# Performance work log

Hardware: AMD Instinct MI355X
Metric: run time of the kernel (lower is better)

The kernel has to match this reference:

```python
import jax, jax.numpy as jnp
import numpy as np

N_ITEMS = 100000
EMBED_DIM = 128
N_SESSIONS = 16384
TOTAL_ITEMS = 819200


def setup_inputs() -> dict:
    key = jax.random.key(0)
    k1, k2, k3 = jax.random.split(key, 3)
    embeddings = jax.random.normal(k1, (N_ITEMS, EMBED_DIM), dtype=jnp.float32)
    item_ids = jax.random.randint(k2, (TOTAL_ITEMS,), 0, N_ITEMS, dtype=jnp.int64)
    segment_ids = jnp.sort(jax.random.randint(k3, (TOTAL_ITEMS,), 0, N_SESSIONS, dtype=jnp.int64))
    return {"embeddings": embeddings, "item_ids": item_ids,
            "segment_ids": segment_ids, "num_sessions": N_SESSIONS}


def reference(embeddings, item_ids, segment_ids, num_sessions):
    # Ragged per-session mean of gathered item embeddings
    gathered = embeddings[item_ids]                      # [total_items, d]
    sums = jax.ops.segment_sum(gathered, segment_ids, num_segments=num_sessions)
    counts = jax.ops.segment_sum(jnp.ones((item_ids.shape[0],), dtype=embeddings.dtype),
                                 segment_ids, num_segments=num_sessions)
    counts = jnp.maximum(counts, 1.0)                    # guard empty sessions
    return sums / counts[:, None]                        # [num_sessions, d]
```

## Files before the change

kernel.cpp:

```cpp
#include <hip/hip_runtime.h>
#include <hip/hip_fp16.h>


constexpr int D = 128;
constexpr int IDS_CAP = 4096;

typedef float f32x2 __attribute__((ext_vector_type(2)));

__global__ void find_starts_diff(const int* __restrict__ seg, int total,
                                 int nsess, int* __restrict__ starts) {
    int j = blockIdx.x * blockDim.x + threadIdx.x;
    if (j >= total) return;
    const int cur  = seg[j];
    const int prev = (j == 0) ? -1 : seg[j - 1];
    for (int s = prev + 1; s <= cur; ++s) starts[s] = j;
    if (j == total - 1) {
        for (int s = cur + 1; s <= nsess; ++s) starts[s] = total;
    }
}

__global__ __launch_bounds__(256)
void repack_kernel(const float* __restrict__ emb, __half* __restrict__ emb2,
                   int nitems) {
    const int item = blockIdx.x * 4 + (threadIdx.x >> 6);
    if (item >= nitems) return;
    const int lane = threadIdx.x & 63;
    const f32x2 v = __builtin_nontemporal_load(
        reinterpret_cast<const f32x2*>(emb + (size_t)item * D) + lane);
    const __half2 h = __floats2half2_rn(v.x, v.y);
    const int g = lane >> 3;
    const int o = lane & 7;
    __half2* dst = reinterpret_cast<__half2*>(
        emb2 + (size_t)g * nitems * 16 + (size_t)item * 16);
    dst[o] = h;
}

__global__ __launch_bounds__(256)
void gather_mean_octet(const __half* __restrict__ emb2,
                       const int* __restrict__ ids,
                       const int* __restrict__ starts,
                       float* __restrict__ out,
                       int nitems, int nsess) {
    __shared__ int lds_ids[IDS_CAP];

    const int g    = blockIdx.x & 7;
    const int s0   = (blockIdx.x >> 3) * 32;
    const int sidx = s0 + (threadIdx.x >> 3);
    const int dl   = threadIdx.x & 7;

    const int sEnd  = (s0 + 32 < nsess) ? s0 + 32 : nsess;
    const int base0 = starts[s0];
    const int range = starts[sEnd] - base0;
    const bool use_lds = (range <= IDS_CAP);

    if (use_lds) {
        for (int t = threadIdx.x; t < range; t += 256)
            lds_ids[t] = ids[base0 + t];
    }
    __syncthreads();

    if (sidx >= nsess) return;

    const int beg = starts[sidx];
    const int len = starts[sidx + 1] - beg;

    const __half* p = emb2 + (size_t)g * nitems * 16 + dl * 2;

    float ax = 0.f, ay = 0.f;

    if (use_lds) {
        const int* idp = lds_ids + (beg - base0);
        int j = 0;
        for (; j + 8 <= len; j += 8) {
            int id[8];
            #pragma unroll
            for (int k = 0; k < 8; ++k) id[k] = idp[j + k];
            float2 f[8];
            #pragma unroll
            for (int k = 0; k < 8; ++k)
                f[k] = __half22float2(
                    *reinterpret_cast<const __half2*>(p + (size_t)id[k] * 16));
            #pragma unroll
            for (int k = 0; k < 8; ++k) { ax += f[k].x; ay += f[k].y; }
        }
        for (; j < len; ++j) {
            const float2 f = __half22float2(
                *reinterpret_cast<const __half2*>(p + (size_t)idp[j] * 16));
            ax += f.x; ay += f.y;
        }
    } else {
        const int* idp = ids + beg;
        int j = 0;
        for (; j + 4 <= len; j += 4) {
            const int i0 = idp[j + 0];
            const int i1 = idp[j + 1];
            const int i2 = idp[j + 2];
            const int i3 = idp[j + 3];
            const float2 f0 = __half22float2(*reinterpret_cast<const __half2*>(p + (size_t)i0 * 16));
            const float2 f1 = __half22float2(*reinterpret_cast<const __half2*>(p + (size_t)i1 * 16));
            const float2 f2 = __half22float2(*reinterpret_cast<const __half2*>(p + (size_t)i2 * 16));
            const float2 f3 = __half22float2(*reinterpret_cast<const __half2*>(p + (size_t)i3 * 16));
            ax += f0.x + f1.x + f2.x + f3.x;
            ay += f0.y + f1.y + f2.y + f3.y;
        }
        for (; j < len; ++j) {
            const float2 f = __half22float2(
                *reinterpret_cast<const __half2*>(p + (size_t)idp[j] * 16));
            ax += f.x; ay += f.y;
        }
    }

    const float inv = (len > 0) ? 1.0f / (float)len : 0.0f;
    f32x2 o = {ax * inv, ay * inv};
    *reinterpret_cast<f32x2*>(out + (size_t)sidx * D + g * 16 + dl * 2) = o;
}

__global__ __launch_bounds__(256)
void seg_mean_kernel(const float* __restrict__ emb,
                     const int* __restrict__ ids,
                     const int* __restrict__ starts,
                     float* __restrict__ out, int nsess) {
    const int tid  = threadIdx.x;
    const int s    = blockIdx.x * 4 + (tid >> 6);
    if (s >= nsess) return;
    const int lane = tid & 63;
    const int gq   = lane >> 5;
    const int l32  = lane & 31;

    const int beg = starts[s];
    const int end = starts[s + 1];

    float4 acc = make_float4(0.f, 0.f, 0.f, 0.f);
    for (int j = beg + gq; j < end; j += 2) {
        const int id = ids[j];
        const float4 v = reinterpret_cast<const float4*>(emb + (size_t)id * D)[l32];
        acc.x += v.x; acc.y += v.y; acc.z += v.z; acc.w += v.w;
    }
    acc.x += __shfl_down(acc.x, 32);
    acc.y += __shfl_down(acc.y, 32);
    acc.z += __shfl_down(acc.z, 32);
    acc.w += __shfl_down(acc.w, 32);
    if (lane < 32) {
        const int cnt = end - beg;
        const float inv = (cnt > 0) ? 1.0f / (float)cnt : 0.0f;
        const float4 o = make_float4(acc.x * inv, acc.y * inv,
                                     acc.z * inv, acc.w * inv);
        reinterpret_cast<float4*>(out + (size_t)s * D)[l32] = o;
    }
}

extern "C" void kernel_launch(void* const* d_in, const int* in_sizes, int n_in,
                              void* d_out, int out_size, void* d_ws, size_t ws_size,
                              hipStream_t stream) {
    const float* emb = (const float*)d_in[0];
    const int*   ids = (const int*)d_in[1];
    const int*   seg = (const int*)d_in[2];
    float*       out = (float*)d_out;

    const int total  = in_sizes[1];
    const int nsess  = out_size / D;
    const int nitems = in_sizes[0] / D;

    const size_t emb2_bytes = (size_t)nitems * D * 2;
    const size_t emb2_pad   = (emb2_bytes + 255) & ~(size_t)255;
    const size_t need       = emb2_pad + (size_t)(nsess + 1) * 4;

    if (ws_size >= need) {
        __half* emb2   = (__half*)d_ws;
        int*    starts = (int*)((char*)d_ws + emb2_pad);

        {
            const int threads = 256;
            const int blocks = (total + threads - 1) / threads;
            find_starts_diff<<<blocks, threads, 0, stream>>>(seg, total, nsess, starts);
        }
        {
            const int blocks = (nitems + 3) / 4;
            repack_kernel<<<blocks, 256, 0, stream>>>(emb, emb2, nitems);
        }
        {
            const int sgroups = (nsess + 31) / 32;
            gather_mean_octet<<<sgroups * 8, 256, 0, stream>>>(emb2, ids, starts,
                                                               out, nitems, nsess);
        }
    } else {
        int* starts = (int*)d_ws;
        {
            const int threads = 256;
            const int blocks = (total + threads - 1) / threads;
            find_starts_diff<<<blocks, threads, 0, stream>>>(seg, total, nsess, starts);
        }
        {
            const int blocks = (nsess + 3) / 4;
            seg_mean_kernel<<<blocks, 256, 0, stream>>>(emb, ids, starts, out, nsess);
        }
    }
}
```

Before: 63.35 us.

## Fuse repack with start-finding and switch gather to 4 column groups of 64 bytes

Merges the fp16 repack and segment-start kernels into one launch whose block range picks the role, removing a launch and letting the two independent preps overlap. The repacked table now has 4 column groups of 32 halves (64 bytes per item row) instead of 8 groups of 16, and the gather uses 16 lanes per session, 16 sessions per block and 4 blocks per session group. Each gathered row segment therefore spans a full 64-byte line. Ids are pre-shifted into byte offsets in LDS, and the LDS cap is halved to match the smaller session group. The trade-off is fewer id reloads per group but fewer blocks and a possibly different cache footprint per block.

```diff
diff --git a/kernel.cpp b/kernel.cpp
--- a/kernel.cpp
+++ b/kernel.cpp
@@ -3,9 +3,105 @@
 
 
 constexpr int D = 128;
-constexpr int IDS_CAP = 4096;
+constexpr int IDS_CAP = 2048;
 
 typedef float f32x2 __attribute__((ext_vector_type(2)));
+
+__global__ __launch_bounds__(256)
+void prep_kernel(const float* __restrict__ emb, __half* __restrict__ emb2,
+                 const int* __restrict__ seg, int* __restrict__ starts,
+                 int nitems, int total, int nsess, int repack_blocks) {
+    if ((int)blockIdx.x < repack_blocks) {
+        const int item = blockIdx.x * 4 + (threadIdx.x >> 6);
+        if (item >= nitems) return;
+        const int lane = threadIdx.x & 63;
+        const f32x2 v = __builtin_nontemporal_load(
+            reinterpret_cast<const f32x2*>(emb + (size_t)item * D) + lane);
+        const __half2 h = __floats2half2_rn(v.x, v.y);
+        const int g = lane >> 4;
+        const int o = lane & 15;
+        __half2* dst = reinterpret_cast<__half2*>(
+            emb2 + (size_t)g * nitems * 32 + (size_t)item * 32);
+        dst[o] = h;
+    } else {
+        const int j = ((int)blockIdx.x - repack_blocks) * 256 + threadIdx.x;
+        if (j >= total) return;
+        const int cur  = seg[j];
+        const int prev = (j == 0) ? -1 : seg[j - 1];
+        for (int s = prev + 1; s <= cur; ++s) starts[s] = j;
+        if (j == total - 1) {
+            for (int s = cur + 1; s <= nsess; ++s) starts[s] = total;
+        }
+    }
+}
+
+__global__ __launch_bounds__(256)
+void gather_mean_hex(const __half* __restrict__ emb2,
+                     const int* __restrict__ ids,
+                     const int* __restrict__ starts,
+                     float* __restrict__ out,
+                     int nitems, int nsess) {
+    __shared__ int lds_off[IDS_CAP];
+
+    const int g    = blockIdx.x & 3;
+    const int s0   = (blockIdx.x >> 2) * 16;
+    const int sidx = s0 + (threadIdx.x >> 4);
+    const int dl   = threadIdx.x & 15;
+
+    const int sEnd  = (s0 + 16 < nsess) ? s0 + 16 : nsess;
+    const int base0 = starts[s0];
+    const int range = starts[sEnd] - base0;
+    const bool use_lds = (range <= IDS_CAP);
+
+    if (use_lds) {
+        for (int t = threadIdx.x; t < range; t += 256)
+            lds_off[t] = ids[base0 + t] << 6;
+    }
+    __syncthreads();
+
+    if (sidx >= nsess) return;
+
+    const int beg = starts[sidx];
+    const int len = starts[sidx + 1] - beg;
+
+    const char* pbase = reinterpret_cast<const char*>(emb2)
+                      + (size_t)g * nitems * 64 + dl * 4;
+
+    float ax = 0.f, ay = 0.f;
+
+    if (use_lds) {
+        const int* offp = lds_off + (beg - base0);
+        int j = 0;
+        for (; j + 8 <= len; j += 8) {
+            int off[8];
+            #pragma unroll
+            for (int k = 0; k < 8; ++k) off[k] = offp[j + k];
+            float2 f[8];
+            #pragma unroll
+            for (int k = 0; k < 8; ++k)
+                f[k] = __half22float2(
+                    *reinterpret_cast<const __half2*>(pbase + (size_t)off[k]));
+            #pragma unroll
+            for (int k = 0; k < 8; ++k) { ax += f[k].x; ay += f[k].y; }
+        }
+        for (; j < len; ++j) {
+            const float2 f = __half22float2(
+                *reinterpret_cast<const __half2*>(pbase + (size_t)offp[j]));
+            ax += f.x; ay += f.y;
+        }
+    } else {
+        const int* idp = ids + beg;
+        for (int j = 0; j < len; ++j) {
+            const float2 f = __half22float2(
+                *reinterpret_cast<const __half2*>(pbase + ((size_t)idp[j] << 6)));
+            ax += f.x; ay += f.y;
+        }
+    }
+
+    const float inv = (len > 0) ? 1.0f / (float)len : 0.0f;
+    f32x2 o = {ax * inv, ay * inv};
+    *reinterpret_cast<f32x2*>(out + (size_t)sidx * D + g * 32 + dl * 2) = o;
+}
 
 __global__ void find_starts_diff(const int* __restrict__ seg, int total,
                                  int nsess, int* __restrict__ starts) {
@@ -17,102 +113,6 @@
     if (j == total - 1) {
         for (int s = cur + 1; s <= nsess; ++s) starts[s] = total;
     }
-}
-
-__global__ __launch_bounds__(256)
-void repack_kernel(const float* __restrict__ emb, __half* __restrict__ emb2,
-                   int nitems) {
-    const int item = blockIdx.x * 4 + (threadIdx.x >> 6);
-    if (item >= nitems) return;
-    const int lane = threadIdx.x & 63;
-    const f32x2 v = __builtin_nontemporal_load(
-        reinterpret_cast<const f32x2*>(emb + (size_t)item * D) + lane);
-    const __half2 h = __floats2half2_rn(v.x, v.y);
-    const int g = lane >> 3;
-    const int o = lane & 7;
-    __half2* dst = reinterpret_cast<__half2*>(
-        emb2 + (size_t)g * nitems * 16 + (size_t)item * 16);
-    dst[o] = h;
-}
-
-__global__ __launch_bounds__(256)
-void gather_mean_octet(const __half* __restrict__ emb2,
-                       const int* __restrict__ ids,
-                       const int* __restrict__ starts,
-                       float* __restrict__ out,
-                       int nitems, int nsess) {
-    __shared__ int lds_ids[IDS_CAP];
-
-    const int g    = blockIdx.x & 7;
-    const int s0   = (blockIdx.x >> 3) * 32;
-    const int sidx = s0 + (threadIdx.x >> 3);
-    const int dl   = threadIdx.x & 7;
-
-    const int sEnd  = (s0 + 32 < nsess) ? s0 + 32 : nsess;
-    const int base0 = starts[s0];
-    const int range = starts[sEnd] - base0;
-    const bool use_lds = (range <= IDS_CAP);
-
-    if (use_lds) {
-        for (int t = threadIdx.x; t < range; t += 256)
-            lds_ids[t] = ids[base0 + t];
-    }
-    __syncthreads();
-
-    if (sidx >= nsess) return;
-
-    const int beg = starts[sidx];
-    const int len = starts[sidx + 1] - beg;
-
-    const __half* p = emb2 + (size_t)g * nitems * 16 + dl * 2;
-
-    float ax = 0.f, ay = 0.f;
-
-    if (use_lds) {
-        const int* idp = lds_ids + (beg - base0);
-        int j = 0;
-        for (; j + 8 <= len; j += 8) {
-            int id[8];
-            #pragma unroll
-            for (int k = 0; k < 8; ++k) id[k] = idp[j + k];
-            float2 f[8];
-            #pragma unroll
-            for (int k = 0; k < 8; ++k)
-                f[k] = __half22float2(
-                    *reinterpret_cast<const __half2*>(p + (size_t)id[k] * 16));
-            #pragma unroll
-            for (int k = 0; k < 8; ++k) { ax += f[k].x; ay += f[k].y; }
-        }
-        for (; j < len; ++j) {
-            const float2 f = __half22float2(
-                *reinterpret_cast<const __half2*>(p + (size_t)idp[j] * 16));
-            ax += f.x; ay += f.y;
-        }
-    } else {
-        const int* idp = ids + beg;
-        int j = 0;
-        for (; j + 4 <= len; j += 4) {
-            const int i0 = idp[j + 0];
-            const int i1 = idp[j + 1];
-            const int i2 = idp[j + 2];
-            const int i3 = idp[j + 3];
-            const float2 f0 = __half22float2(*reinterpret_cast<const __half2*>(p + (size_t)i0 * 16));
-            const float2 f1 = __half22float2(*reinterpret_cast<const __half2*>(p + (size_t)i1 * 16));
-            const float2 f2 = __half22float2(*reinterpret_cast<const __half2*>(p + (size_t)i2 * 16));
-            const float2 f3 = __half22float2(*reinterpret_cast<const __half2*>(p + (size_t)i3 * 16));
-            ax += f0.x + f1.x + f2.x + f3.x;
-            ay += f0.y + f1.y + f2.y + f3.y;
-        }
-        for (; j < len; ++j) {
-            const float2 f = __half22float2(
-                *reinterpret_cast<const __half2*>(p + (size_t)idp[j] * 16));
-            ax += f.x; ay += f.y;
-        }
-    }
-
-    const float inv = (len > 0) ? 1.0f / (float)len : 0.0f;
-    f32x2 o = {ax * inv, ay * inv};
-    *reinterpret_cast<f32x2*>(out + (size_t)sidx * D + g * 16 + dl * 2) = o;
 }
 
 __global__ __launch_bounds__(256)
@@ -170,18 +170,15 @@
         int*    starts = (int*)((char*)d_ws + emb2_pad);
 
         {
-            const int threads = 256;
-            const int blocks = (total + threads - 1) / threads;
-            find_starts_diff<<<blocks, threads, 0, stream>>>(seg, total, nsess, starts);
+            const int repack_blocks = (nitems + 3) / 4;
+            const int starts_blocks = (total + 255) / 256;
+            prep_kernel<<<repack_blocks + starts_blocks, 256, 0, stream>>>(
+                emb, emb2, seg, starts, nitems, total, nsess, repack_blocks);
         }
         {
-            const int blocks = (nitems + 3) / 4;
-            repack_kernel<<<blocks, 256, 0, stream>>>(emb, emb2, nitems);
-        }
-        {
-            const int sgroups = (nsess + 31) / 32;
-            gather_mean_octet<<<sgroups * 8, 256, 0, stream>>>(emb2, ids, starts,
-                                                               out, nitems, nsess);
+            const int sgroups = (nsess + 15) / 16;
+            gather_mean_hex<<<sgroups * 4, 256, 0, stream>>>(emb2, ids, starts,
+                                                             out, nitems, nsess);
         }
     } else {
         int* starts = (int*)d_ws;
```

Result: faster. 55.31 us (-12.7%).
